# Kernel tuning notes

Measured on AMD Instinct MI355X. Metric: run time of the kernel, lower is better.

The kernel has to match this reference:

```python
import jax, jax.numpy as jnp
import numpy as np

EPS = 1e-5

def _ln(x, g, b):
    mu = jnp.mean(x, axis=-1, keepdims=True)
    var = jnp.mean((x - mu) ** 2, axis=-1, keepdims=True)
    return (x - mu) * jax.lax.rsqrt(var + EPS) * g + b

def setup_inputs() -> dict:
    key = jax.random.key(0)
    B, V, I, H = 32, 48, 24, 768
    ks = jax.random.split(key, 10)
    s = 0.02
    return {
        'variables': jax.random.normal(ks[0], (B, V, H), jnp.float32),
        'interventions': jax.random.normal(ks[1], (B, I, H), jnp.float32),
        # variable_encoder: Linear(H,H) + LayerNorm(H)
        'W_enc': jax.random.normal(ks[2], (H, H), jnp.float32) * s,
        'b_enc': jnp.zeros((H,), jnp.float32),
        'g_enc': jnp.ones((H,), jnp.float32),
        'be_enc': jnp.zeros((H,), jnp.float32),
        # graph_generator: Linear(2H,H) + LN(H) + ReLU + Linear(H,1) + Sigmoid
        'Wg1': jax.random.normal(ks[3], (2 * H, H), jnp.float32) * s,
        'bg1': jnp.zeros((H,), jnp.float32),
        'g_g': jnp.ones((H,), jnp.float32),
        'b_g': jnp.zeros((H,), jnp.float32),
        'Wg2': jax.random.normal(ks[4], (H, 1), jnp.float32) * s,
        'bg2': jnp.zeros((1,), jnp.float32),
        # intervention_predictor: Linear(2H,H) + LN(H) + ReLU + Linear(H,H)
        'Wi1': jax.random.normal(ks[5], (2 * H, H), jnp.float32) * s,
        'bi1': jnp.zeros((H,), jnp.float32),
        'g_i': jnp.ones((H,), jnp.float32),
        'b_i': jnp.zeros((H,), jnp.float32),
        'Wi2': jax.random.normal(ks[6], (H, H), jnp.float32) * s,
        'bi2': jnp.zeros((H,), jnp.float32),
    }

def reference(variables, interventions, W_enc, b_enc, g_enc, be_enc,
              Wg1, bg1, g_g, b_g, Wg2, bg2, Wi1, bi1, g_i, b_i, Wi2, bi2):
    H = variables.shape[-1]
    V = variables.shape[1]
    # variable encoder: Linear + LayerNorm + ReLU
    enc = jax.nn.relu(_ln(variables @ W_enc + b_enc, g_enc, be_enc))  # [B,V,H]

    # graph generator over all ordered pairs (i,j): concat([enc_i, enc_j]) @ Wg1
    # split Wg1 so the concat-matmul becomes two small GEMMs + broadcast add
    hi = jnp.einsum('bvh,hk->bvk', enc, Wg1[:H])   # contribution of enc_i
    hj = jnp.einsum('bvh,hk->bvk', enc, Wg1[H:])   # contribution of enc_j
    h = jax.nn.relu(_ln(hi[:, :, None, :] + hj[:, None, :, :] + bg1, g_g, b_g))  # [B,V,V,H]
    score = jax.nn.sigmoid(jnp.squeeze(h @ Wg2, -1) + bg2[0])  # [B,V,V]
    # diagonal (i==j) is never written in the original -> stays zero
    causal_graph = score * (1.0 - jnp.eye(V, dtype=score.dtype))

    # intervention predictor: concat([intervention_i, enc_j]) -> MLP
    ha = jnp.einsum('bih,hk->bik', interventions, Wi1[:H])  # [B,I,H]
    hb = jnp.einsum('bvh,hk->bvk', enc, Wi1[H:])            # [B,V,H]
    h2 = jax.nn.relu(_ln(ha[:, :, None, :] + hb[:, None, :, :] + bi1, g_i, b_i))  # [B,I,V,H]
    effects = h2 @ Wi2 + bi2  # [B,I,V,H]

    return (effects, causal_graph, enc)
```

## Files before the change

### kernel.cpp

```cpp
#include <hip/hip_runtime.h>
#include <math.h>

#define Bp 32
#define Vp 48
#define Ip 24
#define Hp 768
#define EPS 1e-5f

#define EFFECTS_SIZE (Bp*Ip*Vp*Hp)
#define GRAPH_SIZE   (Bp*Vp*Vp)
#define ENC_SIZE     (Bp*Vp*Hp)
#define MS           (Hp*Hp)

typedef __attribute__((ext_vector_type(8))) short short8;
typedef __attribute__((ext_vector_type(4))) float floatx4;
typedef __attribute__((ext_vector_type(2))) float floatx2;
typedef __attribute__((ext_vector_type(4))) unsigned int uintx4;

__device__ __forceinline__ unsigned short f2bf(float f) {
    unsigned int u = __float_as_uint(f);
    u += 0x7fffu + ((u >> 16) & 1u);
    return (unsigned short)(u >> 16);
}
__device__ __forceinline__ unsigned int f2bf2(float a, float b) {
    return (unsigned int)f2bf(a) | ((unsigned int)f2bf(b) << 16);
}

__global__ __launch_bounds__(256) void pack_weights(
    const float* __restrict__ W_enc, const float* __restrict__ Wg1,
    const float* __restrict__ Wi1, const float* __restrict__ Wi2,
    unsigned short* __restrict__ packed)
{
    const int bid = blockIdx.x;
    const int m = bid / 288;
    const int rem = bid - m * 288;
    const int T = rem / 6;
    const int u = rem - T * 6;
    const float* src;
    switch (m) {
        case 0: src = W_enc; break;
        case 1: src = Wg1; break;
        case 2: src = Wg1 + Hp * Hp; break;
        case 3: src = Wi1 + Hp * Hp; break;
        case 4: src = Wi1; break;
        default: src = Wi2; break;
    }
    unsigned short* dst = packed + (size_t)m * MS;
    const int lane = threadIdx.x & 63;
    const int kq = threadIdx.x >> 6;
    const int col = T * 16 + (lane & 15);
    const int krow0 = (lane >> 4) * 8;
    const int kb = kq + 4 * u;
    unsigned int w[4];
#pragma unroll
    for (int p2 = 0; p2 < 4; ++p2) {
        float f0 = src[(size_t)(kb * 32 + krow0 + 2 * p2)     * Hp + col];
        float f1 = src[(size_t)(kb * 32 + krow0 + 2 * p2 + 1) * Hp + col];
        w[p2] = f2bf2(f0, f1);
    }
    uintx4 v; v.x = w[0]; v.y = w[1]; v.z = w[2]; v.w = w[3];
    *(uintx4*)(dst + ((size_t)(T * 24 + kb) * 64 + lane) * 8) = v;
}

__global__ __launch_bounds__(256) void convert_inputs(
    const float* __restrict__ vars, const float* __restrict__ intv,
    const float* __restrict__ bg1, const float* __restrict__ bi1,
    unsigned short* __restrict__ varb, unsigned short* __restrict__ intvb,
    float* __restrict__ bias2304)
{
    const int p = blockIdx.x * 256 + threadIdx.x;
    const int VPn = ENC_SIZE / 2;
    if (p < VPn) {
        float2 f = ((const float2*)vars)[p];
        ((unsigned int*)varb)[p] = f2bf2(f.x, f.y);
    } else {
        int q = p - VPn;
        float2 f = ((const float2*)intv)[q];
        ((unsigned int*)intvb)[q] = f2bf2(f.x, f.y);
    }
    if (blockIdx.x == 0) {
        for (int t = threadIdx.x; t < 2304; t += 256)
            bias2304[t] = (t < 768) ? 0.0f : (t < 1536 ? bg1[t - 768] : bi1[t - 1536]);
    }
}

__global__ __launch_bounds__(256) void gemm32(
    const unsigned short* __restrict__ A, const unsigned short* __restrict__ Bpk,
    const float* __restrict__ bias, float* __restrict__ C, int ldc)
{
    __shared__ unsigned short Asl[2 * 24 * 64 * 8];
    const int tid = threadIdx.x, wave = tid >> 6, lane = tid & 63;
    const int m0 = blockIdx.x * 32;

#pragma unroll
    for (int uu = 0; uu < 12; ++uu) {
        const int s = tid + 256 * uu;
        const int mt = s / 1536;
        const int r2 = s - mt * 1536;
        const int kb = r2 >> 6;
        const int L  = r2 & 63;
        uintx4 v = *(const uintx4*)(A + (size_t)(m0 + mt * 16 + (L & 15)) * Hp
                                      + kb * 32 + (L >> 4) * 8);
        *(uintx4*)(&Asl[((mt * 24 + kb) * 64 + (L ^ (kb & 7))) * 8]) = v;
    }
    __syncthreads();

    const int mrow = lane & 15, kq = lane >> 4;
    const int rot = ((blockIdx.x * 5 + blockIdx.y) & 7) * 3;
    const int wavep = (wave + blockIdx.x) & 3;
    const int Tg0 = blockIdx.y * 12 + wavep * 3;
    const unsigned short* Bbase = Bpk + (size_t)Tg0 * 12288 + lane * 8;

    const floatx4 z = {0.f, 0.f, 0.f, 0.f};
    floatx4 acc[2][3];
#pragma unroll
    for (int mt = 0; mt < 2; ++mt)
#pragma unroll
        for (int nt = 0; nt < 3; ++nt) acc[mt][nt] = z;

    short8 bbuf[4][3], abuf[2][2];
#pragma unroll
    for (int d = 0; d < 3; ++d) {
        int kc = d + rot; if (kc >= 24) kc -= 24;
#pragma unroll
        for (int nt = 0; nt < 3; ++nt)
            bbuf[d][nt] = *(const short8*)(Bbase + (size_t)nt * 12288 + kc * 512);
    }
    {
        int kc = rot;
#pragma unroll
        for (int mt = 0; mt < 2; ++mt)
            abuf[0][mt] = *(const short8*)(&Asl[((mt * 24 + kc) * 64 + (lane ^ (kc & 7))) * 8]);
    }

#pragma unroll
    for (int kb = 0; kb < 24; ++kb) {
        if (kb + 3 < 24) {
            int kc = kb + 3 + rot; if (kc >= 24) kc -= 24;
#pragma unroll
            for (int nt = 0; nt < 3; ++nt)
                bbuf[(kb + 3) & 3][nt] =
                    *(const short8*)(Bbase + (size_t)nt * 12288 + kc * 512);
        }
        if (kb + 1 < 24) {
            int kc = kb + 1 + rot; if (kc >= 24) kc -= 24;
#pragma unroll
            for (int mt = 0; mt < 2; ++mt)
                abuf[(kb + 1) & 1][mt] = *(const short8*)(
                    &Asl[((mt * 24 + kc) * 64 + (lane ^ (kc & 7))) * 8]);
        }
#pragma unroll
        for (int mt = 0; mt < 2; ++mt)
#pragma unroll
            for (int nt = 0; nt < 3; ++nt)
                acc[mt][nt] = __builtin_amdgcn_mfma_f32_16x16x32_bf16(
                    abuf[kb & 1][mt], bbuf[kb & 3][nt], acc[mt][nt], 0, 0, 0);
    }

#pragma unroll
    for (int nt = 0; nt < 3; ++nt) {
        const int colg = (Tg0 + nt) * 16 + mrow;
        const float bv = bias ? bias[colg] : 0.0f;
#pragma unroll
        for (int mt = 0; mt < 2; ++mt)
#pragma unroll
            for (int r = 0; r < 4; ++r)
                C[(size_t)(m0 + mt * 16 + kq * 4 + r) * ldc + colg] = acc[mt][nt][r] + bv;
    }
}

__global__ __launch_bounds__(256) void ln_relu(
    const float* __restrict__ pre, const float* __restrict__ g,
    const float* __restrict__ be, float* __restrict__ encf,
    unsigned short* __restrict__ encb)
{
    const int wave = threadIdx.x >> 6, lane = threadIdx.x & 63;
    const int row = blockIdx.x * 4 + wave;
    const float2* rp = (const float2*)(pre + (size_t)row * Hp);
    float2 x[6]; float s = 0.f, q = 0.f;
#pragma unroll
    for (int c = 0; c < 6; ++c) {
        x[c] = rp[lane + 64 * c];
        s += x[c].x + x[c].y;
        q += x[c].x * x[c].x + x[c].y * x[c].y;
    }
#pragma unroll
    for (int m = 1; m < 64; m <<= 1) { s += __shfl_xor(s, m, 64); q += __shfl_xor(q, m, 64); }
    const float mu = s * (1.0f / Hp);
    const float var = q * (1.0f / Hp) - mu * mu;
    const float rs = rsqrtf(var + EPS);
    floatx2* of = (floatx2*)(encf + (size_t)row * Hp);
    unsigned int* ob = (unsigned int*)(encb + (size_t)row * Hp);
#pragma unroll
    for (int c = 0; c < 6; ++c) {
        const float2 g2 = ((const float2*)g)[lane + 64 * c];
        const float2 b2 = ((const float2*)be)[lane + 64 * c];
        float y0 = fmaxf((x[c].x - mu) * rs * g2.x + b2.x, 0.f);
        float y1 = fmaxf((x[c].y - mu) * rs * g2.y + b2.y, 0.f);
        floatx2 y; y.x = y0; y.y = y1;
        __builtin_nontemporal_store(y, &of[lane + 64 * c]);
        ob[lane + 64 * c] = f2bf2(y0, y1);
    }
}

__global__ __launch_bounds__(256) void graph_kernel(
    const float* __restrict__ ws2, const float* __restrict__ gg_,
    const float* __restrict__ bb_, const float* __restrict__ Wg2,
    const float* __restrict__ bg2, float* __restrict__ out)
{
    const int wave = threadIdx.x >> 6, lane = threadIdx.x & 63;
    const int p = blockIdx.x;
    const int b = p / Vp, i = p - b * Vp;
    const float* hi_row = ws2 + (size_t)p * 2304;
    float ri[12], gg[12], bb[12], w2[12];
#pragma unroll
    for (int c = 0; c < 12; ++c) {
        const int k = lane + 64 * c;
        ri[c] = hi_row[k]; gg[c] = gg_[k]; bb[c] = bb_[k]; w2[c] = Wg2[k];
    }
    const float bg2v = bg2[0];
    const int j0 = wave * 12;
    for (int jj = 0; jj < 12; ++jj) {
        const int j = j0 + jj;
        const float* hj_row = ws2 + (size_t)(b * Vp + j) * 2304 + 768;
        float x[12], s = 0.f, q = 0.f;
#pragma unroll
        for (int c = 0; c < 12; ++c) {
            x[c] = ri[c] + hj_row[lane + 64 * c];
            s += x[c]; q += x[c] * x[c];
        }
#pragma unroll
        for (int m = 1; m < 64; m <<= 1) { s += __shfl_xor(s, m, 64); q += __shfl_xor(q, m, 64); }
        const float mu = s * (1.0f / Hp);
        const float var = q * (1.0f / Hp) - mu * mu;
        const float rs = rsqrtf(var + EPS);
        float pd = 0.f;
#pragma unroll
        for (int c = 0; c < 12; ++c) {
            float y = fmaxf((x[c] - mu) * rs * gg[c] + bb[c], 0.f);
            pd = fmaf(y, w2[c], pd);
        }
#pragma unroll
        for (int m = 1; m < 64; m <<= 1) pd += __shfl_xor(pd, m, 64);
        if (lane == 0) {
            float sc = (i == j) ? 0.0f : 1.0f / (1.0f + expf(-(pd + bg2v)));
            out[(size_t)p * Vp + j] = sc;
        }
    }
}

__global__ __launch_bounds__(256) void effects48(
    const float* __restrict__ ha, const float* __restrict__ ws2,
    const float* __restrict__ g_i, const float* __restrict__ b_i,
    const unsigned short* __restrict__ Bpk, const float* __restrict__ bi2,
    float* __restrict__ out)
{
    __shared__ unsigned short Asl[3 * 24 * 64 * 8];
    const int tid = threadIdx.x, wave = tid >> 6, lane = tid & 63;
    const int bi = blockIdx.x;
    const int b = bi / Ip;
    const int half = lane >> 5, hl = lane & 31;

    const floatx4* hap = (const floatx4*)(ha + (size_t)bi * Hp);
    const floatx4* gp = (const floatx4*)g_i;
    const floatx4* bp = (const floatx4*)b_i;
    floatx4 hav[6], gv[6], bv[6];
#pragma unroll
    for (int t = 0; t < 3; ++t) {
        hav[2*t]   = hap[2*hl + 64*t];     hav[2*t+1] = hap[2*hl + 1 + 64*t];
        gv[2*t]    = gp[2*hl + 64*t];      gv[2*t+1]  = gp[2*hl + 1 + 64*t];
        bv[2*t]    = bp[2*hl + 64*t];      bv[2*t+1]  = bp[2*hl + 1 + 64*t];
    }

#pragma unroll
    for (int p = 0; p < 6; ++p) {
        const int u = wave * 12 + 2 * p + half;
        const floatx4* hbp = (const floatx4*)(ws2 + (size_t)(b * Vp + u) * 2304 + 1536);
        floatx4 x[6]; float s = 0.f, q = 0.f;
#pragma unroll
        for (int t = 0; t < 3; ++t) {
            x[2*t]   = hav[2*t]   + hbp[2*hl + 64*t];
            x[2*t+1] = hav[2*t+1] + hbp[2*hl + 1 + 64*t];
        }
#pragma unroll
        for (int c = 0; c < 6; ++c) {
            s += x[c].x + x[c].y + x[c].z + x[c].w;
            q += x[c].x*x[c].x + x[c].y*x[c].y + x[c].z*x[c].z + x[c].w*x[c].w;
        }
#pragma unroll
        for (int m = 1; m < 32; m <<= 1) { s += __shfl_xor(s, m, 64); q += __shfl_xor(q, m, 64); }
        const float mu = s * (1.0f / Hp);
        const float var = q * (1.0f / Hp) - mu * mu;
        const float rs = rsqrtf(var + EPS);
        const int mt = u >> 4, mrow = u & 15;
#pragma unroll
        for (int t = 0; t < 3; ++t) {
            float y0 = fmaxf((x[2*t].x   - mu) * rs * gv[2*t].x   + bv[2*t].x,   0.f);
            float y1 = fmaxf((x[2*t].y   - mu) * rs * gv[2*t].y   + bv[2*t].y,   0.f);
            float y2 = fmaxf((x[2*t].z   - mu) * rs * gv[2*t].z   + bv[2*t].z,   0.f);
            float y3 = fmaxf((x[2*t].w   - mu) * rs * gv[2*t].w   + bv[2*t].w,   0.f);
            float y4 = fmaxf((x[2*t+1].x - mu) * rs * gv[2*t+1].x + bv[2*t+1].x, 0.f);
            float y5 = fmaxf((x[2*t+1].y - mu) * rs * gv[2*t+1].y + bv[2*t+1].y, 0.f);
            float y6 = fmaxf((x[2*t+1].z - mu) * rs * gv[2*t+1].z + bv[2*t+1].z, 0.f);
            float y7 = fmaxf((x[2*t+1].w - mu) * rs * gv[2*t+1].w + bv[2*t+1].w, 0.f);
            const int cpk = hl + 32 * t;
            const int kb = cpk >> 2, kq2 = cpk & 3;
            const int phys = (mt * 24 + kb) * 64 + ((kq2 * 16 + mrow) ^ (kb & 7));
            uintx4 v;
            v.x = f2bf2(y0, y1); v.y = f2bf2(y2, y3);
            v.z = f2bf2(y4, y5); v.w = f2bf2(y6, y7);
            *(uintx4*)(&Asl[phys * 8]) = v;
        }
    }
    __syncthreads();

    const int mrow = lane & 15, kq = lane >> 4;
    const int rot = (bi & 7) * 3;
    const int wavep = (wave + bi) & 3;
    const floatx4 z = {0.f, 0.f, 0.f, 0.f};
#pragma unroll
    for (int G = 0; G < 2; ++G) {
        const int Tg0 = wavep * 12 + G * 6;
        const unsigned short* Bbase = Bpk + (size_t)Tg0 * 12288 + lane * 8;
        floatx4 acc[3][6];
#pragma unroll
        for (int mt = 0; mt < 3; ++mt)
#pragma unroll
            for (int nt = 0; nt < 6; ++nt) acc[mt][nt] = z;

        short8 bbuf[4][6], abuf[2][3];
#pragma unroll
        for (int d = 0; d < 3; ++d) {
            int kc = d + rot; if (kc >= 24) kc -= 24;
#pragma unroll
            for (int nt = 0; nt < 6; ++nt)
                bbuf[d][nt] = *(const short8*)(Bbase + (size_t)nt * 12288 + kc * 512);
        }
        {
            int kc = rot;
#pragma unroll
            for (int mt = 0; mt < 3; ++mt)
                abuf[0][mt] = *(const short8*)(&Asl[((mt * 24 + kc) * 64 + (lane ^ (kc & 7))) * 8]);
        }

#pragma unroll
        for (int kb = 0; kb < 24; ++kb) {
            if (kb + 3 < 24) {
                int kc = kb + 3 + rot; if (kc >= 24) kc -= 24;
#pragma unroll
                for (int nt = 0; nt < 6; ++nt)
                    bbuf[(kb + 3) & 3][nt] =
                        *(const short8*)(Bbase + (size_t)nt * 12288 + kc * 512);
            }
            if (kb + 1 < 24) {
                int kc = kb + 1 + rot; if (kc >= 24) kc -= 24;
#pragma unroll
                for (int mt = 0; mt < 3; ++mt)
                    abuf[(kb + 1) & 1][mt] = *(const short8*)(
                        &Asl[((mt * 24 + kc) * 64 + (lane ^ (kc & 7))) * 8]);
            }
            __builtin_amdgcn_s_setprio(1);
#pragma unroll
            for (int mt = 0; mt < 3; ++mt)
#pragma unroll
                for (int nt = 0; nt < 6; ++nt)
                    acc[mt][nt] = __builtin_amdgcn_mfma_f32_16x16x32_bf16(
                        abuf[kb & 1][mt], bbuf[kb & 3][nt], acc[mt][nt], 0, 0, 0);
            __builtin_amdgcn_s_setprio(0);
        }

#pragma unroll
        for (int nt = 0; nt < 6; ++nt) {
            const int colg = (Tg0 + nt) * 16 + mrow;
            const float biasv = bi2[colg];
#pragma unroll
            for (int mt = 0; mt < 3; ++mt) {
#pragma unroll
                for (int r = 0; r < 4; ++r) {
                    __builtin_nontemporal_store(
                        acc[mt][nt][r] + biasv,
                        &out[(size_t)(bi * 48 + mt * 16 + kq * 4 + r) * Hp + colg]);
                }
            }
        }
    }
}

extern "C" void kernel_launch(void* const* d_in, const int* in_sizes, int n_in,
                              void* d_out, int out_size, void* d_ws, size_t ws_size,
                              hipStream_t stream) {
    const float* variables     = (const float*)d_in[0];
    const float* interventions = (const float*)d_in[1];
    const float* W_enc  = (const float*)d_in[2];
    const float* b_enc  = (const float*)d_in[3];
    const float* g_enc  = (const float*)d_in[4];
    const float* be_enc = (const float*)d_in[5];
    const float* Wg1 = (const float*)d_in[6];
    const float* bg1 = (const float*)d_in[7];
    const float* g_g = (const float*)d_in[8];
    const float* b_g = (const float*)d_in[9];
    const float* Wg2 = (const float*)d_in[10];
    const float* bg2 = (const float*)d_in[11];
    const float* Wi1 = (const float*)d_in[12];
    const float* bi1 = (const float*)d_in[13];
    const float* g_i = (const float*)d_in[14];
    const float* b_i = (const float*)d_in[15];
    const float* Wi2 = (const float*)d_in[16];
    const float* bi2 = (const float*)d_in[17];

    float* out = (float*)d_out;
    float* effects = out;
    float* graph = out + EFFECTS_SIZE;
    float* enc_f = out + EFFECTS_SIZE + GRAPH_SIZE;

    char* wsb = (char*)d_ws;
    unsigned short* packedW = (unsigned short*)wsb;
    float* ws2  = (float*)(wsb + 7077888);
    float* pre1 = ws2;
    float* ha   = (float*)(wsb + 7077888 + 14155776);
    unsigned short* varb  = (unsigned short*)(wsb + 23592960);
    unsigned short* intvb = (unsigned short*)(wsb + 25952256);
    unsigned short* encb  = (unsigned short*)(wsb + 27131904);
    float* bias2304 = (float*)(wsb + 29491200);

    pack_weights<<<1728, 256, 0, stream>>>(W_enc, Wg1, Wi1, Wi2, packedW);
    convert_inputs<<<3456, 256, 0, stream>>>(variables, interventions, bg1, bi1,
                                             varb, intvb, bias2304);
    gemm32<<<dim3(48, 4), 256, 0, stream>>>(varb, packedW, b_enc, pre1, Hp);
    ln_relu<<<384, 256, 0, stream>>>(pre1, g_enc, be_enc, enc_f, encb);
    gemm32<<<dim3(48, 12), 256, 0, stream>>>(encb, packedW + (size_t)1 * MS,
                                             bias2304, ws2, 2304);
    gemm32<<<dim3(24, 4), 256, 0, stream>>>(intvb, packedW + (size_t)4 * MS,
                                            nullptr, ha, Hp);
    graph_kernel<<<Bp * Vp, 256, 0, stream>>>(ws2, g_g, b_g, Wg2, bg2, graph);
    effects48<<<Bp * Ip, 256, 0, stream>>>(ha, ws2, g_i, b_i,
                                           packedW + (size_t)5 * MS, bi2, effects);
}
```

Measured before the change: 293.4 us.

## Retile effects GEMM to 96-row blocks over two interventions with 8 waves

The effects kernel now has each 512-thread block handle two intervention rows (96 M-rows) and half of the N dimension, so each B-weight fragment loaded from global memory feeds six M tiles instead of three. The LN prologue computes both interventions' rows together and shares the hb loads between them. The graph kernel is vectorised with float4 loads and processes two j columns per iteration, and the small GEMM gets MFMA priority hints. In exchange the kernel uses twice the LDS per block and more accumulator registers, which may limit occupancy.

After: 279.4 us. 4.8% less time.

```diff
diff --git a/kernel.cpp b/kernel.cpp
--- a/kernel.cpp
+++ b/kernel.cpp
@@ -24,6 +24,23 @@
 }
 __device__ __forceinline__ unsigned int f2bf2(float a, float b) {
     return (unsigned int)f2bf(a) | ((unsigned int)f2bf(b) << 16);
+}
+
+__device__ __forceinline__ uintx4 ln8(floatx4 xa, floatx4 xb, float mu, float rs,
+                                      floatx4 ga, floatx4 gb, floatx4 ba, floatx4 bb)
+{
+    float y0 = fmaxf((xa.x - mu) * rs * ga.x + ba.x, 0.f);
+    float y1 = fmaxf((xa.y - mu) * rs * ga.y + ba.y, 0.f);
+    float y2 = fmaxf((xa.z - mu) * rs * ga.z + ba.z, 0.f);
+    float y3 = fmaxf((xa.w - mu) * rs * ga.w + ba.w, 0.f);
+    float y4 = fmaxf((xb.x - mu) * rs * gb.x + bb.x, 0.f);
+    float y5 = fmaxf((xb.y - mu) * rs * gb.y + bb.y, 0.f);
+    float y6 = fmaxf((xb.z - mu) * rs * gb.z + bb.z, 0.f);
+    float y7 = fmaxf((xb.w - mu) * rs * gb.w + bb.w, 0.f);
+    uintx4 v;
+    v.x = f2bf2(y0, y1); v.y = f2bf2(y2, y3);
+    v.z = f2bf2(y4, y5); v.w = f2bf2(y6, y7);
+    return v;
 }
 
 __global__ __launch_bounds__(256) void pack_weights(
@@ -149,12 +166,14 @@
                 abuf[(kb + 1) & 1][mt] = *(const short8*)(
                     &Asl[((mt * 24 + kc) * 64 + (lane ^ (kc & 7))) * 8]);
         }
+        __builtin_amdgcn_s_setprio(1);
 #pragma unroll
         for (int mt = 0; mt < 2; ++mt)
 #pragma unroll
             for (int nt = 0; nt < 3; ++nt)
                 acc[mt][nt] = __builtin_amdgcn_mfma_f32_16x16x32_bf16(
                     abuf[kb & 1][mt], bbuf[kb & 3][nt], acc[mt][nt], 0, 0, 0);
+        __builtin_amdgcn_s_setprio(0);
     }
 
 #pragma unroll
@@ -211,176 +230,213 @@
     const int wave = threadIdx.x >> 6, lane = threadIdx.x & 63;
     const int p = blockIdx.x;
     const int b = p / Vp, i = p - b * Vp;
-    const float* hi_row = ws2 + (size_t)p * 2304;
-    float ri[12], gg[12], bb[12], w2[12];
-#pragma unroll
-    for (int c = 0; c < 12; ++c) {
+    const floatx4* hi4 = (const floatx4*)(ws2 + (size_t)p * 2304);
+    const floatx4* gg4 = (const floatx4*)gg_;
+    const floatx4* bb4 = (const floatx4*)bb_;
+    const floatx4* w24 = (const floatx4*)Wg2;
+    floatx4 ri[3], gg[3], bb[3], w2[3];
+#pragma unroll
+    for (int c = 0; c < 3; ++c) {
         const int k = lane + 64 * c;
-        ri[c] = hi_row[k]; gg[c] = gg_[k]; bb[c] = bb_[k]; w2[c] = Wg2[k];
+        ri[c] = hi4[k]; gg[c] = gg4[k]; bb[c] = bb4[k]; w2[c] = w24[k];
     }
     const float bg2v = bg2[0];
     const int j0 = wave * 12;
-    for (int jj = 0; jj < 12; ++jj) {
-        const int j = j0 + jj;
-        const float* hj_row = ws2 + (size_t)(b * Vp + j) * 2304 + 768;
-        float x[12], s = 0.f, q = 0.f;
-#pragma unroll
-        for (int c = 0; c < 12; ++c) {
-            x[c] = ri[c] + hj_row[lane + 64 * c];
-            s += x[c]; q += x[c] * x[c];
-        }
-#pragma unroll
-        for (int m = 1; m < 64; m <<= 1) { s += __shfl_xor(s, m, 64); q += __shfl_xor(q, m, 64); }
-        const float mu = s * (1.0f / Hp);
-        const float var = q * (1.0f / Hp) - mu * mu;
-        const float rs = rsqrtf(var + EPS);
-        float pd = 0.f;
-#pragma unroll
-        for (int c = 0; c < 12; ++c) {
-            float y = fmaxf((x[c] - mu) * rs * gg[c] + bb[c], 0.f);
-            pd = fmaf(y, w2[c], pd);
-        }
-#pragma unroll
-        for (int m = 1; m < 64; m <<= 1) pd += __shfl_xor(pd, m, 64);
+    for (int jj = 0; jj < 12; jj += 2) {
+        const int jA = j0 + jj, jB = jA + 1;
+        const floatx4* hjA = (const floatx4*)(ws2 + (size_t)(b * Vp + jA) * 2304 + 768);
+        const floatx4* hjB = (const floatx4*)(ws2 + (size_t)(b * Vp + jB) * 2304 + 768);
+        floatx4 xA[3], xB[3];
+        float sA = 0.f, qA = 0.f, sB = 0.f, qB = 0.f;
+#pragma unroll
+        for (int c = 0; c < 3; ++c) {
+            const int k = lane + 64 * c;
+            xA[c] = ri[c] + hjA[k];
+            xB[c] = ri[c] + hjB[k];
+            sA += xA[c].x + xA[c].y + xA[c].z + xA[c].w;
+            qA += xA[c].x * xA[c].x + xA[c].y * xA[c].y + xA[c].z * xA[c].z + xA[c].w * xA[c].w;
+            sB += xB[c].x + xB[c].y + xB[c].z + xB[c].w;
+            qB += xB[c].x * xB[c].x + xB[c].y * xB[c].y + xB[c].z * xB[c].z + xB[c].w * xB[c].w;
+        }
+#pragma unroll
+        for (int m = 1; m < 64; m <<= 1) {
+            sA += __shfl_xor(sA, m, 64); qA += __shfl_xor(qA, m, 64);
+            sB += __shfl_xor(sB, m, 64); qB += __shfl_xor(qB, m, 64);
+        }
+        const float muA = sA * (1.0f / Hp);
+        const float rsA = rsqrtf(qA * (1.0f / Hp) - muA * muA + EPS);
+        const float muB = sB * (1.0f / Hp);
+        const float rsB = rsqrtf(qB * (1.0f / Hp) - muB * muB + EPS);
+        float pdA = 0.f, pdB = 0.f;
+#pragma unroll
+        for (int c = 0; c < 3; ++c) {
+            float yA0 = fmaxf((xA[c].x - muA) * rsA * gg[c].x + bb[c].x, 0.f);
+            float yA1 = fmaxf((xA[c].y - muA) * rsA * gg[c].y + bb[c].y, 0.f);
+            float yA2 = fmaxf((xA[c].z - muA) * rsA * gg[c].z + bb[c].z, 0.f);
+            float yA3 = fmaxf((xA[c].w - muA) * rsA * gg[c].w + bb[c].w, 0.f);
+            pdA = fmaf(yA0, w2[c].x, pdA); pdA = fmaf(yA1, w2[c].y, pdA);
+            pdA = fmaf(yA2, w2[c].z, pdA); pdA = fmaf(yA3, w2[c].w, pdA);
+            float yB0 = fmaxf((xB[c].x - muB) * rsB * gg[c].x + bb[c].x, 0.f);
+            float yB1 = fmaxf((xB[c].y - muB) * rsB * gg[c].y + bb[c].y, 0.f);
+            float yB2 = fmaxf((xB[c].z - muB) * rsB * gg[c].z + bb[c].z, 0.f);
+            float yB3 = fmaxf((xB[c].w - muB) * rsB * gg[c].w + bb[c].w, 0.f);
+            pdB = fmaf(yB0, w2[c].x, pdB); pdB = fmaf(yB1, w2[c].y, pdB);
+            pdB = fmaf(yB2, w2[c].z, pdB); pdB = fmaf(yB3, w2[c].w, pdB);
+        }
+#pragma unroll
+        for (int m = 1; m < 64; m <<= 1) {
+            pdA += __shfl_xor(pdA, m, 64);
+            pdB += __shfl_xor(pdB, m, 64);
+        }
         if (lane == 0) {
-            float sc = (i == j) ? 0.0f : 1.0f / (1.0f + expf(-(pd + bg2v)));
-            out[(size_t)p * Vp + j] = sc;
-        }
-    }
-}
-
-__global__ __launch_bounds__(256) void effects48(
+            float scA = (i == jA) ? 0.0f : 1.0f / (1.0f + expf(-(pdA + bg2v)));
+            float scB = (i == jB) ? 0.0f : 1.0f / (1.0f + expf(-(pdB + bg2v)));
+            out[(size_t)p * Vp + jA] = scA;
+            out[(size_t)p * Vp + jB] = scB;
+        }
+    }
+}
+
+__global__ __launch_bounds__(512, 2) void effects96(
     const float* __restrict__ ha, const float* __restrict__ ws2,
     const float* __restrict__ g_i, const float* __restrict__ b_i,
     const unsigned short* __restrict__ Bpk, const float* __restrict__ bi2,
     float* __restrict__ out)
 {
-    __shared__ unsigned short Asl[3 * 24 * 64 * 8];
+    __shared__ unsigned short Asl[6 * 24 * 64 * 8];
     const int tid = threadIdx.x, wave = tid >> 6, lane = tid & 63;
-    const int bi = blockIdx.x;
-    const int b = bi / Ip;
+    const int bid = blockIdx.x;
+    const int pair = bid >> 1, nhalf = bid & 1;
+    const int b = pair / 12;
+    const int bi0 = b * Ip + (pair - b * 12) * 2;
     const int half = lane >> 5, hl = lane & 31;
 
-    const floatx4* hap = (const floatx4*)(ha + (size_t)bi * Hp);
-    const floatx4* gp = (const floatx4*)g_i;
-    const floatx4* bp = (const floatx4*)b_i;
-    floatx4 hav[6], gv[6], bv[6];
-#pragma unroll
-    for (int t = 0; t < 3; ++t) {
-        hav[2*t]   = hap[2*hl + 64*t];     hav[2*t+1] = hap[2*hl + 1 + 64*t];
-        gv[2*t]    = gp[2*hl + 64*t];      gv[2*t+1]  = gp[2*hl + 1 + 64*t];
-        bv[2*t]    = bp[2*hl + 64*t];      bv[2*t+1]  = bp[2*hl + 1 + 64*t];
-    }
-
-#pragma unroll
-    for (int p = 0; p < 6; ++p) {
-        const int u = wave * 12 + 2 * p + half;
-        const floatx4* hbp = (const floatx4*)(ws2 + (size_t)(b * Vp + u) * 2304 + 1536);
-        floatx4 x[6]; float s = 0.f, q = 0.f;
+    {
+        const floatx4* ha0 = (const floatx4*)(ha + (size_t)bi0 * Hp);
+        const floatx4* ha1 = (const floatx4*)(ha + (size_t)(bi0 + 1) * Hp);
+        const floatx4* gp = (const floatx4*)g_i;
+        const floatx4* bp = (const floatx4*)b_i;
+        floatx4 hv0[6], hv1[6], gv[6], bv[6];
 #pragma unroll
         for (int t = 0; t < 3; ++t) {
-            x[2*t]   = hav[2*t]   + hbp[2*hl + 64*t];
-            x[2*t+1] = hav[2*t+1] + hbp[2*hl + 1 + 64*t];
-        }
-#pragma unroll
-        for (int c = 0; c < 6; ++c) {
-            s += x[c].x + x[c].y + x[c].z + x[c].w;
-            q += x[c].x*x[c].x + x[c].y*x[c].y + x[c].z*x[c].z + x[c].w*x[c].w;
-        }
-#pragma unroll
-        for (int m = 1; m < 32; m <<= 1) { s += __shfl_xor(s, m, 64); q += __shfl_xor(q, m, 64); }
-        const float mu = s * (1.0f / Hp);
-        const float var = q * (1.0f / Hp) - mu * mu;
-        const float rs = rsqrtf(var + EPS);
-        const int mt = u >> 4, mrow = u & 15;
-#pragma unroll
-        for (int t = 0; t < 3; ++t) {
-            float y0 = fmaxf((x[2*t].x   - mu) * rs * gv[2*t].x   + bv[2*t].x,   0.f);
-            float y1 = fmaxf((x[2*t].y   - mu) * rs * gv[2*t].y   + bv[2*t].y,   0.f);
-            float y2 = fmaxf((x[2*t].z   - mu) * rs * gv[2*t].z   + bv[2*t].z,   0.f);
-            float y3 = fmaxf((x[2*t].w   - mu) * rs * gv[2*t].w   + bv[2*t].w,   0.f);
-            float y4 = fmaxf((x[2*t+1].x - mu) * rs * gv[2*t+1].x + bv[2*t+1].x, 0.f);
-            float y5 = fmaxf((x[2*t+1].y - mu) * rs * gv[2*t+1].y + bv[2*t+1].y, 0.f);
-            float y6 = fmaxf((x[2*t+1].z - mu) * rs * gv[2*t+1].z + bv[2*t+1].z, 0.f);
-            float y7 = fmaxf((x[2*t+1].w - mu) * rs * gv[2*t+1].w + bv[2*t+1].w, 0.f);
-            const int cpk = hl + 32 * t;
-            const int kb = cpk >> 2, kq2 = cpk & 3;
-            const int phys = (mt * 24 + kb) * 64 + ((kq2 * 16 + mrow) ^ (kb & 7));
-            uintx4 v;
-            v.x = f2bf2(y0, y1); v.y = f2bf2(y2, y3);
-            v.z = f2bf2(y4, y5); v.w = f2bf2(y6, y7);
-            *(uintx4*)(&Asl[phys * 8]) = v;
+            hv0[2*t] = ha0[2*hl + 64*t];  hv0[2*t+1] = ha0[2*hl + 1 + 64*t];
+            hv1[2*t] = ha1[2*hl + 64*t];  hv1[2*t+1] = ha1[2*hl + 1 + 64*t];
+            gv[2*t]  = gp[2*hl + 64*t];   gv[2*t+1]  = gp[2*hl + 1 + 64*t];
+            bv[2*t]  = bp[2*hl + 64*t];   bv[2*t+1]  = bp[2*hl + 1 + 64*t];
+        }
+
+#pragma unroll
+        for (int p = 0; p < 3; ++p) {
+            const int j = wave * 6 + 2 * p + half;
+            const floatx4* hbp = (const floatx4*)(ws2 + (size_t)(b * Vp + j) * 2304 + 1536);
+            floatx4 x0[6], x1[6];
+            float s0 = 0.f, q0 = 0.f, s1 = 0.f, q1 = 0.f;
+#pragma unroll
+            for (int t = 0; t < 3; ++t) {
+                const floatx4 hA = hbp[2*hl + 64*t];
+                const floatx4 hB = hbp[2*hl + 1 + 64*t];
+                x0[2*t]   = hv0[2*t]   + hA;  x0[2*t+1] = hv0[2*t+1] + hB;
+                x1[2*t]   = hv1[2*t]   + hA;  x1[2*t+1] = hv1[2*t+1] + hB;
+            }
+#pragma unroll
+            for (int c = 0; c < 6; ++c) {
+                s0 += x0[c].x + x0[c].y + x0[c].z + x0[c].w;
+                q0 += x0[c].x*x0[c].x + x0[c].y*x0[c].y + x0[c].z*x0[c].z + x0[c].w*x0[c].w;
+                s1 += x1[c].x + x1[c].y + x1[c].z + x1[c].w;
+                q1 += x1[c].x*x1[c].x + x1[c].y*x1[c].y + x1[c].z*x1[c].z + x1[c].w*x1[c].w;
+            }
+#pragma unroll
+            for (int m = 1; m < 32; m <<= 1) {
+                s0 += __shfl_xor(s0, m, 64); q0 += __shfl_xor(q0, m, 64);
+                s1 += __shfl_xor(s1, m, 64); q1 += __shfl_xor(q1, m, 64);
+            }
+            const float mu0 = s0 * (1.0f / Hp);
+            const float rs0 = rsqrtf(q0 * (1.0f / Hp) - mu0 * mu0 + EPS);
+            const float mu1 = s1 * (1.0f / Hp);
+            const float rs1 = rsqrtf(q1 * (1.0f / Hp) - mu1 * mu1 + EPS);
+            const int mt0 = j >> 4, mt1 = 3 + mt0, mr = j & 15;
+#pragma unroll
+            for (int t = 0; t < 3; ++t) {
+                const int cpk = hl + 32 * t;
+                const int kb = cpk >> 2, kq2 = cpk & 3;
+                const int swz = (kq2 * 16 + mr) ^ (kb & 7);
+                uintx4 v0 = ln8(x0[2*t], x0[2*t+1], mu0, rs0,
+                                gv[2*t], gv[2*t+1], bv[2*t], bv[2*t+1]);
+                *(uintx4*)(&Asl[((mt0 * 24 + kb) * 64 + swz) * 8]) = v0;
+                uintx4 v1 = ln8(x1[2*t], x1[2*t+1], mu1, rs1,
+                                gv[2*t], gv[2*t+1], bv[2*t], bv[2*t+1]);
+                *(uintx4*)(&Asl[((mt1 * 24 + kb) * 64 + swz) * 8]) = v1;
+            }
         }
     }
     __syncthreads();
 
     const int mrow = lane & 15, kq = lane >> 4;
-    const int rot = (bi & 7) * 3;
-    const int wavep = (wave + bi) & 3;
+    const int rot = (pair & 7) * 3;
+    const int wavep = (wave + pair) & 7;
+    const int Tg0 = nhalf * 24 + wavep * 3;
+    const unsigned short* Bbase = Bpk + (size_t)Tg0 * 12288 + lane * 8;
+
     const floatx4 z = {0.f, 0.f, 0.f, 0.f};
-#pragma unroll
-    for (int G = 0; G < 2; ++G) {
-        const int Tg0 = wavep * 12 + G * 6;
-        const unsigned short* Bbase = Bpk + (size_t)Tg0 * 12288 + lane * 8;
-        floatx4 acc[3][6];
-#pragma unroll
-        for (int mt = 0; mt < 3; ++mt)
-#pragma unroll
-            for (int nt = 0; nt < 6; ++nt) acc[mt][nt] = z;
-
-        short8 bbuf[4][6], abuf[2][3];
-#pragma unroll
-        for (int d = 0; d < 3; ++d) {
-            int kc = d + rot; if (kc >= 24) kc -= 24;
-#pragma unroll
-            for (int nt = 0; nt < 6; ++nt)
-                bbuf[d][nt] = *(const short8*)(Bbase + (size_t)nt * 12288 + kc * 512);
-        }
-        {
-            int kc = rot;
-#pragma unroll
-            for (int mt = 0; mt < 3; ++mt)
-                abuf[0][mt] = *(const short8*)(&Asl[((mt * 24 + kc) * 64 + (lane ^ (kc & 7))) * 8]);
-        }
-
-#pragma unroll
-        for (int kb = 0; kb < 24; ++kb) {
-            if (kb + 3 < 24) {
-                int kc = kb + 3 + rot; if (kc >= 24) kc -= 24;
-#pragma unroll
-                for (int nt = 0; nt < 6; ++nt)
-                    bbuf[(kb + 3) & 3][nt] =
-                        *(const short8*)(Bbase + (size_t)nt * 12288 + kc * 512);
-            }
-            if (kb + 1 < 24) {
-                int kc = kb + 1 + rot; if (kc >= 24) kc -= 24;
-#pragma unroll
-                for (int mt = 0; mt < 3; ++mt)
-                    abuf[(kb + 1) & 1][mt] = *(const short8*)(
-                        &Asl[((mt * 24 + kc) * 64 + (lane ^ (kc & 7))) * 8]);
-            }
-            __builtin_amdgcn_s_setprio(1);
-#pragma unroll
-            for (int mt = 0; mt < 3; ++mt)
-#pragma unroll
-                for (int nt = 0; nt < 6; ++nt)
-                    acc[mt][nt] = __builtin_amdgcn_mfma_f32_16x16x32_bf16(
-                        abuf[kb & 1][mt], bbuf[kb & 3][nt], acc[mt][nt], 0, 0, 0);
-            __builtin_amdgcn_s_setprio(0);
-        }
-
-#pragma unroll
-        for (int nt = 0; nt < 6; ++nt) {
-            const int colg = (Tg0 + nt) * 16 + mrow;
-            const float biasv = bi2[colg];
-#pragma unroll
-            for (int mt = 0; mt < 3; ++mt) {
-#pragma unroll
-                for (int r = 0; r < 4; ++r) {
-                    __builtin_nontemporal_store(
-                        acc[mt][nt][r] + biasv,
-                        &out[(size_t)(bi * 48 + mt * 16 + kq * 4 + r) * Hp + colg]);
-                }
+    floatx4 acc[6][3];
+#pragma unroll
+    for (int mt = 0; mt < 6; ++mt)
+#pragma unroll
+        for (int nt = 0; nt < 3; ++nt) acc[mt][nt] = z;
+
+    short8 bbuf[4][3], abuf[2][6];
+#pragma unroll
+    for (int d = 0; d < 3; ++d) {
+        int kc = d + rot; if (kc >= 24) kc -= 24;
+#pragma unroll
+        for (int nt = 0; nt < 3; ++nt)
+            bbuf[d][nt] = *(const short8*)(Bbase + (size_t)nt * 12288 + kc * 512);
+    }
+    {
+        int kc = rot;
+#pragma unroll
+        for (int mt = 0; mt < 6; ++mt)
+            abuf[0][mt] = *(const short8*)(&Asl[((mt * 24 + kc) * 64 + (lane ^ (kc & 7))) * 8]);
+    }
+
+#pragma unroll
+    for (int kb = 0; kb < 24; ++kb) {
+        if (kb + 3 < 24) {
+            int kc = kb + 3 + rot; if (kc >= 24) kc -= 24;
+#pragma unroll
+            for (int nt = 0; nt < 3; ++nt)
+                bbuf[(kb + 3) & 3][nt] =
+                    *(const short8*)(Bbase + (size_t)nt * 12288 + kc * 512);
+        }
+        if (kb + 1 < 24) {
+            int kc = kb + 1 + rot; if (kc >= 24) kc -= 24;
+#pragma unroll
+            for (int mt = 0; mt < 6; ++mt)
+                abuf[(kb + 1) & 1][mt] = *(const short8*)(
+                    &Asl[((mt * 24 + kc) * 64 + (lane ^ (kc & 7))) * 8]);
+        }
+        __builtin_amdgcn_s_setprio(1);
+#pragma unroll
+        for (int mt = 0; mt < 6; ++mt)
+#pragma unroll
+            for (int nt = 0; nt < 3; ++nt)
+                acc[mt][nt] = __builtin_amdgcn_mfma_f32_16x16x32_bf16(
+                    abuf[kb & 1][mt], bbuf[kb & 3][nt], acc[mt][nt], 0, 0, 0);
+        __builtin_amdgcn_s_setprio(0);
+    }
+
+#pragma unroll
+    for (int nt = 0; nt < 3; ++nt) {
+        const int colg = (Tg0 + nt) * 16 + mrow;
+        const float biasv = bi2[colg];
+#pragma unroll
+        for (int mt = 0; mt < 6; ++mt) {
+#pragma unroll
+            for (int r = 0; r < 4; ++r) {
+                const int rr = mt * 16 + kq * 4 + r;
+                __builtin_nontemporal_store(
+                    acc[mt][nt][r] + biasv,
+                    &out[(size_t)(bi0 * 48 + rr) * Hp + colg]);
             }
         }
     }
@@ -433,6 +489,6 @@
     gemm32<<<dim3(24, 4), 256, 0, stream>>>(intvb, packedW + (size_t)4 * MS,
                                             nullptr, ha, Hp);
     graph_kernel<<<Bp * Vp, 256, 0, stream>>>(ws2, g_g, b_g, Wg2, bg2, graph);
-    effects48<<<Bp * Ip, 256, 0, stream>>>(ha, ws2, g_i, b_i,
-                                           packedW + (size_t)5 * MS, bi2, effects);
-}
+    effects96<<<768, 512, 0, stream>>>(ha, ws2, g_i, b_i,
+                                       packedW + (size_t)5 * MS, bi2, effects);
+}
```
